# Kernel optimization log

Measured on AMD Instinct MI355X. Metric: run time of the kernel, lower is better.

Reference implementation:

```python
import jax, jax.numpy as jnp
import numpy as np
from jax import lax

B, N, FIN, T = 16, 1024, 32, 24
K, CC, CT = 3, 64, 64   # cheb order, nb_chev_filter, nb_time_filter
EPS = 1e-5


def setup_inputs() -> dict:
    key = jax.random.key(0)
    ks = jax.random.split(key, 16)
    g = lambda i, shape, sc=1.0: jax.random.normal(ks[i], shape, jnp.float32) * sc
    return dict(
        x=g(0, (B, N, FIN, T)),
        # spatial attention params
        W1=g(1, (T,), 0.1), W2=g(2, (FIN, T), 0.1), W3=g(3, (FIN,), 0.1),
        # temporal attention params
        U1=g(4, (N,), 0.03), U2=g(5, (FIN, N), 0.03), U3=g(6, (FIN,), 0.1),
        # Chebyshev polynomials T_k (K,N,N) and Theta (K,F_in,C_chev)
        cheb=g(7, (K, N, N), 1.0 / np.sqrt(N)),
        Theta=g(8, (K, FIN, CC), 1.0 / np.sqrt(FIN)),
        # time conv (1,3) stride (1,1) pad (0,1), residual conv (1,1)
        tc_w=g(9, (CT, CC, 1, 3), 1.0 / np.sqrt(3 * CC)), tc_b=g(10, (CT,), 0.01),
        rc_w=g(11, (CT, FIN, 1, 1), 1.0 / np.sqrt(FIN)), rc_b=g(12, (CT,), 0.01),
        gamma=jnp.ones((CT,), jnp.float32), beta=jnp.zeros((CT,), jnp.float32),
    )


def _layer_norm(z, gamma, beta):
    mu = jnp.mean(z, axis=-1, keepdims=True)
    var = jnp.mean(jnp.square(z - mu), axis=-1, keepdims=True)
    return (z - mu) * lax.rsqrt(var + EPS) * gamma + beta


def reference(x, W1, W2, W3, U1, U2, U3, cheb, Theta, tc_w, tc_b, rc_w, rc_b, gamma, beta):
    # ---- temporal attention: (B,T,T), softmax over axis=1 (as in torch dim=1)
    lhs_t = jnp.einsum('bnft,n->btf', x, U1) @ U2            # (B,T,N)
    rhs_t = jnp.einsum('f,bnft->bnt', U3, x)                 # (B,N,T)
    E = jax.nn.softmax(jnp.einsum('btn,bns->bts', lhs_t, rhs_t), axis=1)  # (B,T,T)

    # x_TAt = reshape(B,N*F,T) @ E, reshaped back
    x_TAt = jnp.einsum('bnft,bts->bnfs', x, E)               # (B,N,F,T)

    # ---- spatial attention on x_TAt: (B,N,N), softmax over axis=1
    lhs_s = jnp.einsum('bnft,t->bnf', x_TAt, W1) @ W2        # (B,N,T)
    rhs_s = jnp.einsum('f,bnft->btn', W3, x_TAt)             # (B,T,N)
    S = jax.nn.softmax(jnp.einsum('bnt,btm->bnm', lhs_s, rhs_s), axis=1)  # (B,N,N)

    # ---- K-order Chebyshev graph conv with spatial attention, fused over T and K
    # rhs[k,b,m,f,t] = sum_n (T_k[n,m]*S[b,n,m]) * x[b,n,f,t]
    Tk_at = cheb[:, None] * S[None]                          # (K,B,N,N)
    rhs = jnp.einsum('kbnm,bnft->kbmft', Tk_at, x)           # (K,B,N,F,T)
    spatial_gcn = jax.nn.relu(jnp.einsum('kbmft,kfo->bmot', rhs, Theta))  # (B,N,CC,T)

    # ---- time conv (1,3) pad (0,1) on (B,CC,N,T)
    dn = ('NCHW', 'OIHW', 'NCHW')
    tco = lax.conv_general_dilated(spatial_gcn.transpose(0, 2, 1, 3), tc_w,
                                   window_strides=(1, 1), padding=[(0, 0), (1, 1)],
                                   dimension_numbers=dn) + tc_b[None, :, None, None]
    # ---- residual 1x1 conv on (B,F,N,T)
    res = lax.conv_general_dilated(x.transpose(0, 2, 1, 3), rc_w,
                                   window_strides=(1, 1), padding=[(0, 0), (0, 0)],
                                   dimension_numbers=dn) + rc_b[None, :, None, None]

    z = jax.nn.relu(res + tco)                               # (B,CT,N,T)
    z = _layer_norm(z.transpose(0, 3, 2, 1), gamma, beta)    # (B,T,N,CT), LN over CT
    return z.transpose(0, 2, 3, 1)                           # (B,N,CT,T)
```

## Files before the change

### kernel.cpp

```cpp
#include <hip/hip_runtime.h>
#include <hip/hip_bf16.h>
#include <math.h>


namespace {

constexpr int B = 16, N = 1024, F = 32, T = 24, CC = 64, CT = 64;
constexpr int FT = F * T;
constexpr int CTT = CT * T;
constexpr int NSEG = 8;

using f32x4  = __attribute__((ext_vector_type(4))) float;
using short8 = __attribute__((ext_vector_type(8))) short;

__device__ __forceinline__ float b2f(__hip_bfloat16 v) { return __bfloat162float(v); }
__device__ __forceinline__ unsigned short f2bu(float x) {
  union { float f; unsigned u; } c; c.f = x;
  unsigned u = c.u;
  return (unsigned short)((u + 0x7FFFu + ((u >> 16) & 1u)) >> 16);
}
__device__ __forceinline__ float us2f(unsigned short u) {
  union { unsigned u; float f; } c; c.u = ((unsigned)u) << 16; return c.f;
}
__device__ __forceinline__ void gload16(const void* g, void* l) {
  __builtin_amdgcn_global_load_lds(
      (const __attribute__((address_space(1))) unsigned int*)g,
      (__attribute__((address_space(3))) unsigned int*)l, 16, 0, 0);
}

__global__ void k_lhs_t(const float* x, const float* U1, float* lhst) {
  int bi = blockIdx.x;
  int f = bi % F; int t = (bi / F) % T; int b = bi / (F * T);
  int tid = threadIdx.x;
  float acc = 0.f;
  for (int n = tid; n < N; n += 64)
    acc += x[(((size_t)b * N + n) * F + f) * T + t] * U1[n];
  #pragma unroll
  for (int off = 32; off > 0; off >>= 1) acc += __shfl_down(acc, off);
  if (tid == 0) lhst[bi] = acc;
}

__global__ void k_lhs2(const float* lhst, const float* U2, float* lhs2) {
  __shared__ float ls[F];
  int tid = threadIdx.x;
  int id = blockIdx.x * 256 + tid;
  int n = id % N; int bt = id / N;
  if (tid < F) ls[tid] = lhst[bt * F + tid];
  __syncthreads();
  float acc = 0.f;
  #pragma unroll
  for (int f = 0; f < F; ++f) acc += ls[f] * U2[f * N + n];
  lhs2[id] = acc;
}

__global__ void k_fx(const float* x, const float* U3, const float* W3,
                     float* rhst, float* w3x) {
  __shared__ float u3s[F], w3s[F];
  int tid = threadIdx.x;
  if (tid < F) { u3s[tid] = U3[tid]; w3s[tid] = W3[tid]; }
  __syncthreads();
  int id = blockIdx.x * 256 + tid;
  int t = id % T; int bn = id / T;
  float au = 0.f, aw = 0.f;
  #pragma unroll
  for (int f = 0; f < F; ++f) {
    float v = x[((size_t)bn * F + f) * T + t];
    au += u3s[f] * v; aw += w3s[f] * v;
  }
  rhst[id] = au; w3x[id] = aw;
}

__global__ void k_Elog(const float* lhs2, const float* rhst, float* Elog) {
  int bi = blockIdx.x;
  int s = bi % T; int t = (bi / T) % T; int b = bi / (T * T);
  int tid = threadIdx.x;
  float acc = 0.f;
  for (int n = tid; n < N; n += 64)
    acc += lhs2[(b * T + t) * N + n] * rhst[(b * N + n) * T + s];
  #pragma unroll
  for (int off = 32; off > 0; off >>= 1) acc += __shfl_down(acc, off);
  if (tid == 0) Elog[bi] = acc;
}

__global__ void k_Esm(const float* Elog, float* E) {
  int b = blockIdx.x; int s = threadIdx.x;
  if (s >= T) return;
  float mx = -1e30f;
  for (int t = 0; t < T; ++t) mx = fmaxf(mx, Elog[(b * T + t) * T + s]);
  float sum = 0.f;
  for (int t = 0; t < T; ++t) sum += expf(Elog[(b * T + t) * T + s] - mx);
  float inv = 1.f / sum;
  for (int t = 0; t < T; ++t)
    E[(b * T + t) * T + s] = expf(Elog[(b * T + t) * T + s] - mx) * inv;
}

__global__ void k_EW1(const float* E, const float* W1, float* EW1) {
  int b = blockIdx.x; int t = threadIdx.x;
  if (t >= T) return;
  float acc = 0.f;
  for (int s = 0; s < T; ++s) acc += E[(b * T + t) * T + s] * W1[s];
  EW1[b * T + t] = acc;
}

__global__ void k_tmp1x(const float* x, const float* EW1, float* tmp1) {
  __shared__ float ew[T];
  int tid = threadIdx.x;
  int id = blockIdx.x * 256 + tid;
  int b = id / (N * F);
  if (tid < T) ew[tid] = EW1[b * T + tid];
  __syncthreads();
  const float* xr = x + (size_t)id * T;
  float acc = 0.f;
  #pragma unroll
  for (int t = 0; t < T; ++t) acc += xr[t] * ew[t];
  tmp1[id] = acc;
}

__global__ void k_lhs_s(const float* tmp1, const float* W2, float* lhss) {
  int id = blockIdx.x * 256 + threadIdx.x;
  int t = id % T; int bn = id / T;
  float acc = 0.f;
  #pragma unroll
  for (int f = 0; f < F; ++f) acc += tmp1[bn * F + f] * W2[f * T + t];
  lhss[id] = acc;
}

__global__ void k_rhss(const float* w3x, const float* E, float* rhss) {
  __shared__ float Ec[T];
  int tid = threadIdx.x;
  int id = blockIdx.x * 256 + tid;
  int m = id % N; int t = (id / N) % T; int b = id / (N * T);
  if (tid < T) Ec[tid] = E[(b * T + tid) * T + t];
  __syncthreads();
  const float* wr = w3x + ((size_t)b * N + m) * T;
  float acc = 0.f;
  #pragma unroll
  for (int tp = 0; tp < T; ++tp) acc += wr[tp] * Ec[tp];
  rhss[id] = acc;
}

__global__ void k_Slog(const float* lhss, const float* rhss, __hip_bfloat16* S) {
  __shared__ float rt[T][256];
  __shared__ float lt[16][T];
  int m0 = blockIdx.x * 256, n0 = blockIdx.y * 16, b = blockIdx.z;
  int tid = threadIdx.x;
  for (int t = 0; t < T; ++t) rt[t][tid] = rhss[((size_t)b * T + t) * N + m0 + tid];
  for (int i = tid; i < 16 * T; i += 256) {
    int n = i / T, t = i % T;
    lt[n][t] = lhss[((size_t)b * N + n0 + n) * T + t];
  }
  __syncthreads();
  #pragma unroll 4
  for (int n = 0; n < 16; ++n) {
    float acc = 0.f;
    #pragma unroll
    for (int t = 0; t < T; ++t) acc += lt[n][t] * rt[t][tid];
    S[((size_t)b * N + n0 + n) * N + m0 + tid] = __float2bfloat16(acc);
  }
}

__global__ __launch_bounds__(256) void k_Ssum(const __hip_bfloat16* S,
                                              float* pmx, float* psm) {
  int m0 = blockIdx.x * 128; int b = blockIdx.y; int z = blockIdx.z;
  int tid = threadIdx.x;
  int lane = tid & 63, nq = tid >> 6;
  int c = m0 + lane * 2;
  float mx0 = -1e30f, sm0 = 0.f, mx1 = -1e30f, sm1 = 0.f;
  #pragma unroll 4
  for (int i = 0; i < 32; ++i) {
    int n = z * 128 + i * 4 + nq;
    unsigned u = *(const unsigned*)&S[((size_t)b * N + n) * N + c];
    float v0 = us2f((unsigned short)(u & 0xffffu));
    float v1 = us2f((unsigned short)(u >> 16));
    float nm0 = fmaxf(mx0, v0);
    sm0 = sm0 * __expf(mx0 - nm0) + __expf(v0 - nm0); mx0 = nm0;
    float nm1 = fmaxf(mx1, v1);
    sm1 = sm1 * __expf(mx1 - nm1) + __expf(v1 - nm1); mx1 = nm1;
  }
  __shared__ float lmx[4][128], lsm[4][128];
  lmx[nq][lane * 2] = mx0; lmx[nq][lane * 2 + 1] = mx1;
  lsm[nq][lane * 2] = sm0; lsm[nq][lane * 2 + 1] = sm1;
  __syncthreads();
  if (nq == 0) {
    #pragma unroll
    for (int cc2 = 0; cc2 < 2; ++cc2) {
      int col = lane * 2 + cc2;
      float M = lmx[0][col], Sg = lsm[0][col];
      #pragma unroll
      for (int s = 1; s < 4; ++s) {
        float m2 = lmx[s][col], s2 = lsm[s][col];
        float nm = fmaxf(M, m2);
        Sg = Sg * __expf(M - nm) + s2 * __expf(m2 - nm);
        M = nm;
      }
      pmx[((size_t)z * B + b) * N + m0 + col] = M;
      psm[((size_t)z * B + b) * N + m0 + col] = Sg;
    }
  }
}

__global__ void k_Scomb(const float* pmx, const float* psm,
                        float* smax, float* sinv) {
  int id = blockIdx.x * 256 + threadIdx.x;
  float M = -1e30f, Sg = 0.f;
  #pragma unroll
  for (int z = 0; z < NSEG; ++z) {
    float m2 = pmx[(size_t)z * B * N + id];
    float s2 = psm[(size_t)z * B * N + id];
    float nm = fmaxf(M, m2);
    Sg = Sg * __expf(M - nm) + s2 * __expf(m2 - nm);
    M = nm;
  }
  smax[id] = M;
  sinv[id] = 1.f / Sg;
}

__global__ __launch_bounds__(256) void k_prepA(const float* cheb,
                                               const __hip_bfloat16* S,
                                               const float* smax,
                                               const float* sinv,
                                               unsigned short* Abf,
                                               int Bc, int b0) {
  __shared__ float Tl[64][65];
  int z = blockIdx.z;
  int k = z / Bc, bl = z % Bc, b = b0 + bl;
  int n0 = blockIdx.x * 64, m0 = blockIdx.y * 64;
  int tid = threadIdx.x;
  int j = tid & 63, i4 = tid >> 6;
  float cm = smax[(size_t)b * N + m0 + j];
  float ci = sinv[(size_t)b * N + m0 + j];
  #pragma unroll
  for (int it = 0; it < 16; ++it) {
    int i = it * 4 + i4;
    Tl[i][j] = cheb[((size_t)k * N + n0 + i) * N + m0 + j] *
               (__expf(b2f(S[((size_t)b * N + n0 + i) * N + m0 + j]) - cm) * ci);
  }
  __syncthreads();
  int i2 = (tid & 31) * 2, j8 = tid >> 5;
  #pragma unroll
  for (int it = 0; it < 8; ++it) {
    int jj = it * 8 + j8;
    unsigned u = (unsigned)f2bu(Tl[i2][jj]) | ((unsigned)f2bu(Tl[i2 + 1][jj]) << 16);
    *(unsigned*)&Abf[((size_t)z * N + m0 + jj) * N + n0 + i2] = u;
  }
}

__global__ __launch_bounds__(256) void k_prepX(const float* x, unsigned short* xT,
                                               int b0) {
  __shared__ float Tl[64][65];
  int bl = blockIdx.z, b = b0 + bl;
  int n0 = blockIdx.x * 64, c0 = blockIdx.y * 64;
  int tid = threadIdx.x;
  int j = tid & 63, i4 = tid >> 6;
  #pragma unroll
  for (int it = 0; it < 16; ++it) {
    int i = it * 4 + i4;
    Tl[i][j] = x[((size_t)b * N + n0 + i) * FT + c0 + j];
  }
  __syncthreads();
  int i2 = (tid & 31) * 2, j8 = tid >> 5;
  #pragma unroll
  for (int it = 0; it < 8; ++it) {
    int jj = it * 8 + j8;
    int c = c0 + jj;
    int row = (c % 24) * 32 + c / 24;
    unsigned u = (unsigned)f2bu(Tl[i2][jj]) | ((unsigned)f2bu(Tl[i2 + 1][jj]) << 16);
    *(unsigned*)&xT[((size_t)bl * FT + row) * N + n0 + i2] = u;
  }
}

__global__ void k_prepW(const float* Theta, const float* tcw, const float* rcw,
                        unsigned short* wbf) {
  int tid = threadIdx.x;
  for (int g = tid; g < 64 * 96; g += 256) {
    int o = g / 96, kk = g % 96;
    wbf[g] = f2bu(Theta[kk * 64 + o]);
  }
  for (int g = tid; g < 64 * 192; g += 256) {
    int o = g / 192, r = g % 192;
    int jj = r / 64, cc = r % 64;
    wbf[6144 + g] = f2bu(tcw[o * 192 + cc * 3 + jj]);
  }
  for (int g = tid; g < 32 * 64; g += 256) {
    int f = g >> 6, o = g & 63;
    wbf[18432 + (f >> 1) * 128 + o * 2 + (f & 1)] = f2bu(rcw[o * 32 + f]);
  }
}

__global__ __launch_bounds__(256) void k_gemm3(const unsigned short* Abf,
                                               const unsigned short* xT,
                                               float* rk, size_t kstride,
                                               int Bc) {
  __shared__ __align__(16) unsigned short A_l[3 * 64 * 64];
  __shared__ __align__(16) unsigned short X_l[128 * 64];
  int bl = blockIdx.z;
  int m0 = blockIdx.y * 64, c0 = blockIdx.x * 128;
  int tid = threadIdx.x;
  int lane = tid & 63, w = tid >> 6;
  int l15 = lane & 15, quad = lane >> 4;
  int wmi = w & 1, wci = w >> 1;
  int nh = lane & 7, ml = lane >> 3;
  int swz = nh ^ ml;

  f32x4 acc[3][2][4];
  #pragma unroll
  for (int k = 0; k < 3; ++k)
    #pragma unroll
    for (int mt = 0; mt < 2; ++mt)
      #pragma unroll
      for (int ct = 0; ct < 4; ++ct) acc[k][mt][ct] = (f32x4){0.f, 0.f, 0.f, 0.f};

  for (int n0 = 0; n0 < N; n0 += 64) {
    #pragma unroll
    for (int it = 0; it < 6; ++it) {
      int k = it >> 1, mh = it & 1;
      int rowb = mh * 32 + w * 8;
      gload16(&Abf[((size_t)(k * Bc + bl) * N + m0 + rowb + ml) * N + n0 + swz * 8],
              &A_l[(k * 64 + rowb) * 64]);
    }
    #pragma unroll
    for (int it = 0; it < 4; ++it) {
      int cb = it * 32 + w * 8;
      gload16(&xT[((size_t)bl * FT + c0 + cb + ml) * N + n0 + swz * 8],
              &X_l[cb * 64]);
    }
    __syncthreads();
    #pragma unroll
    for (int ks = 0; ks < 2; ++ks) {
      short8 bfr[4];
      #pragma unroll
      for (int ct = 0; ct < 4; ++ct) {
        int row = wci * 64 + ct * 16 + l15;
        int pc = (ks * 4 + quad) ^ (row & 7);
        bfr[ct] = *(const short8*)&X_l[row * 64 + pc * 8];
      }
      #pragma unroll
      for (int k = 0; k < 3; ++k)
        #pragma unroll
        for (int mt = 0; mt < 2; ++mt) {
          int row = wmi * 32 + mt * 16 + l15;
          int pc = (ks * 4 + quad) ^ (row & 7);
          short8 af = *(const short8*)&A_l[(k * 64 + row) * 64 + pc * 8];
          #pragma unroll
          for (int ct = 0; ct < 4; ++ct)
            acc[k][mt][ct] = __builtin_amdgcn_mfma_f32_16x16x32_bf16(
                af, bfr[ct], acc[k][mt][ct], 0, 0, 0);
        }
    }
    __syncthreads();
  }
  #pragma unroll
  for (int k = 0; k < 3; ++k)
    #pragma unroll
    for (int mt = 0; mt < 2; ++mt)
      #pragma unroll
      for (int ct = 0; ct < 4; ++ct) {
        int col = c0 + wci * 64 + ct * 16 + l15;
        #pragma unroll
        for (int r = 0; r < 4; ++r) {
          int row = m0 + wmi * 32 + mt * 16 + quad * 4 + r;
          rk[k * kstride + ((size_t)bl * N + row) * FT + col] = acc[k][mt][ct][r];
        }
      }
}

__global__ __launch_bounds__(256) void k_fuse(const float* rk, size_t kstride,
                                              const float* x,
                                              const unsigned short* wbf,
                                              const float* tcb, const float* rcb,
                                              const float* gam, const float* bet,
                                              float* out, int b0) {
  __shared__ __align__(16) unsigned char smem[38272];
  unsigned short* A_l = (unsigned short*)smem;
  float* co_l = (float*)(smem + 13312);
  int tid = threadIdx.x;
  int w = tid >> 6, lane = tid & 63;
  int l15 = lane & 15, quad = lane >> 4;
  int r0l = blockIdx.x * 4;
  int o0 = w * 16;

  short8 bth[3], btc[6];
  {
    int o = o0 + l15;
    #pragma unroll
    for (int ks = 0; ks < 3; ++ks)
      bth[ks] = *(const short8*)&wbf[o * 96 + ks * 32 + quad * 8];
    #pragma unroll
    for (int s = 0; s < 6; ++s)
      btc[s] = *(const short8*)&wbf[6144 + o * 192 + s * 32 + quad * 8];
  }

  #pragma unroll
  for (int it = 0; it < 9; ++it) {
    int ch = it * 256 + tid;
    int k = ch / 768, r2 = ch % 768;
    int m = r2 / 192, r3 = r2 % 192;
    int t = r3 >> 3, fq = r3 & 7;
    const float4 v = *(const float4*)&rk[(size_t)k * kstride +
        (size_t)(r0l + m) * FT + t * 32 + fq * 4];
    unsigned long long pk = (unsigned long long)f2bu(v.x) |
        ((unsigned long long)f2bu(v.y) << 16) |
        ((unsigned long long)f2bu(v.z) << 32) |
        ((unsigned long long)f2bu(v.w) << 48);
    *(unsigned long long*)&A_l[(m * 24 + t) * 104 + k * 32 + fq * 4] = pk;
  }
  __syncthreads();

  f32x4 th[6];
  #pragma unroll
  for (int Mt = 0; Mt < 6; ++Mt) {
    th[Mt] = (f32x4){0.f, 0.f, 0.f, 0.f};
    #pragma unroll
    for (int ks = 0; ks < 3; ++ks) {
      short8 af = *(const short8*)&A_l[(Mt * 16 + l15) * 104 + ks * 32 + quad * 8];
      th[Mt] = __builtin_amdgcn_mfma_f32_16x16x32_bf16(af, bth[ks], th[Mt], 0, 0, 0);
    }
  }
  __syncthreads();

  #pragma unroll
  for (int e = tid; e < 512; e += 256) {
    int m = e >> 7, rr = (e >> 6) & 1, cc = e & 63;
    int rp = m * 26 + rr * 25;
    *(unsigned short*)(smem + rp * 128 + ((cc * 2) ^ ((rp & 7) << 4))) = 0;
  }
  #pragma unroll
  for (int Mt = 0; Mt < 6; ++Mt)
    #pragma unroll
    for (int r = 0; r < 4; ++r) {
      int row = Mt * 16 + quad * 4 + r;
      int m = row / 24, t = row % 24;
      int rp = m * 26 + t + 1;
      int cc = o0 + l15;
      *(unsigned short*)(smem + rp * 128 + ((cc * 2) ^ ((rp & 7) << 4))) =
          f2bu(fmaxf(th[Mt][r], 0.f));
    }
  __syncthreads();

  f32x4 cv[6];
  #pragma unroll
  for (int Mt = 0; Mt < 6; ++Mt) {
    int row = Mt * 16 + l15;
    int m = row / 24, t = row % 24;
    cv[Mt] = (f32x4){0.f, 0.f, 0.f, 0.f};
    #pragma unroll
    for (int s = 0; s < 6; ++s) {
      int rp = m * 26 + t + (s >> 1);
      int cb = (32 * (s & 1) + quad * 8) * 2;
      short8 af = *(const short8*)(smem + rp * 128 + (cb ^ ((rp & 7) << 4)));
      cv[Mt] = __builtin_amdgcn_mfma_f32_16x16x32_bf16(af, btc[s], cv[Mt], 0, 0, 0);
    }
  }
  #pragma unroll
  for (int Mt = 0; Mt < 6; ++Mt)
    #pragma unroll
    for (int r = 0; r < 4; ++r) {
      int row = Mt * 16 + quad * 4 + r;
      co_l[row * 65 + o0 + l15] = cv[Mt][r];
    }
  __syncthreads();

  int o = lane;
  float bias = tcb[o] + rcb[o];
  float acc[T];
  #pragma unroll
  for (int t = 0; t < T; ++t) acc[t] = co_l[(w * 24 + t) * 65 + o] + bias;

  size_t grow = (size_t)b0 * N + r0l + w;
  const float* xrow = x + grow * FT;
  const unsigned* rcp = (const unsigned*)(wbf + 18432);
  #pragma unroll 4
  for (int f2 = 0; f2 < 16; ++f2) {
    unsigned u = rcp[f2 * 64 + o];
    float wf0 = us2f((unsigned short)(u & 0xffffu));
    float wf1 = us2f((unsigned short)(u >> 16));
    const float4* xp0 = (const float4*)&xrow[(f2 * 2) * 24];
    const float4* xp1 = (const float4*)&xrow[(f2 * 2 + 1) * 24];
    #pragma unroll
    for (int q = 0; q < 6; ++q) {
      float4 v0 = xp0[q], v1 = xp1[q];
      acc[q * 4 + 0] += wf0 * v0.x + wf1 * v1.x;
      acc[q * 4 + 1] += wf0 * v0.y + wf1 * v1.y;
      acc[q * 4 + 2] += wf0 * v0.z + wf1 * v1.z;
      acc[q * 4 + 3] += wf0 * v0.w + wf1 * v1.w;
    }
  }
  float g = gam[o], be = bet[o];
  #pragma unroll
  for (int t = 0; t < T; ++t) {
    float z = fmaxf(acc[t], 0.f);
    float s = z, q = z * z;
    #pragma unroll
    for (int off = 1; off < 64; off <<= 1) {
      s += __shfl_xor(s, off);
      q += __shfl_xor(q, off);
    }
    float mu = s * (1.f / 64.f);
    float var = q * (1.f / 64.f) - mu * mu;
    acc[t] = (z - mu) * rsqrtf(var + 1e-5f) * g + be;
  }
  float* orow = out + grow * CTT + o * T;
  #pragma unroll
  for (int q = 0; q < 6; ++q)
    ((float4*)orow)[q] =
        make_float4(acc[q * 4], acc[q * 4 + 1], acc[q * 4 + 2], acc[q * 4 + 3]);
}

}

extern "C" void kernel_launch(void* const* d_in, const int* in_sizes, int n_in,
                              void* d_out, int out_size, void* d_ws, size_t ws_size,
                              hipStream_t stream) {
  (void)in_sizes; (void)n_in; (void)out_size;
  const float* x     = (const float*)d_in[0];
  const float* W1    = (const float*)d_in[1];
  const float* W2    = (const float*)d_in[2];
  const float* W3    = (const float*)d_in[3];
  const float* U1    = (const float*)d_in[4];
  const float* U2    = (const float*)d_in[5];
  const float* U3    = (const float*)d_in[6];
  const float* cheb  = (const float*)d_in[7];
  const float* Theta = (const float*)d_in[8];
  const float* tcw   = (const float*)d_in[9];
  const float* tcb   = (const float*)d_in[10];
  const float* rcw   = (const float*)d_in[11];
  const float* rcb   = (const float*)d_in[12];
  const float* gam   = (const float*)d_in[13];
  const float* bet   = (const float*)d_in[14];
  float* out = (float*)d_out;

  const size_t SB_BYTES = (size_t)B * N * N * 2;
  const size_t WB_BYTES = 65536;
  const size_t AB_PER_B = (size_t)3 * N * N * 2;
  const size_t XT_PER_B = (size_t)FT * N * 2;
  const size_t RK_PER_B = (size_t)3 * N * FT * 4;
  const size_t SMALL = 2816384 * 4;
  int Bc = 16;
  while (Bc > 1 && SB_BYTES + WB_BYTES + SMALL +
             (size_t)Bc * (AB_PER_B + XT_PER_B + RK_PER_B) > ws_size)
    Bc >>= 1;

  char* w = (char*)d_ws;
  __hip_bfloat16* Sb = (__hip_bfloat16*)w;
  unsigned short* wbf = (unsigned short*)(w + SB_BYTES);
  unsigned short* Abf = (unsigned short*)(w + SB_BYTES + WB_BYTES);
  unsigned short* xTb = (unsigned short*)(w + SB_BYTES + WB_BYTES +
                                          (size_t)Bc * AB_PER_B);
  float* rkbuf = (float*)(w + SB_BYTES + WB_BYTES +
                          (size_t)Bc * (AB_PER_B + XT_PER_B));
  size_t kstride = (size_t)Bc * N * FT;
  float* sm = (float*)(w + SB_BYTES + WB_BYTES +
                       (size_t)Bc * (AB_PER_B + XT_PER_B + RK_PER_B));
  float* lhst = sm;
  float* lhs2 = lhst + B * T * F;
  float* rhst = lhs2 + B * T * N;
  float* w3x  = rhst + B * N * T;
  float* Elog = w3x + B * N * T;
  float* E    = Elog + B * T * T;
  float* EW1  = E + B * T * T;
  float* tmp1 = EW1 + B * T;
  float* lhss = tmp1 + B * N * F;
  float* rhss = lhss + B * N * T;
  float* pmx  = rhss + B * N * T;
  float* psm  = pmx + NSEG * B * N;
  float* smax = psm + NSEG * B * N;
  float* sinv = smax + B * N;

  k_lhs_t<<<B * T * F, 64, 0, stream>>>(x, U1, lhst);
  k_lhs2<<<(B * T * N) / 256, 256, 0, stream>>>(lhst, U2, lhs2);
  k_fx<<<(B * N * T) / 256, 256, 0, stream>>>(x, U3, W3, rhst, w3x);
  k_Elog<<<B * T * T, 64, 0, stream>>>(lhs2, rhst, Elog);
  k_Esm<<<B, 64, 0, stream>>>(Elog, E);
  k_EW1<<<B, 64, 0, stream>>>(E, W1, EW1);

  k_tmp1x<<<(B * N * F) / 256, 256, 0, stream>>>(x, EW1, tmp1);
  k_lhs_s<<<(B * N * T) / 256, 256, 0, stream>>>(tmp1, W2, lhss);
  k_rhss<<<(B * N * T) / 256, 256, 0, stream>>>(w3x, E, rhss);
  k_Slog<<<dim3(N / 256, N / 16, B), 256, 0, stream>>>(lhss, rhss, Sb);
  k_Ssum<<<dim3(N / 128, B, NSEG), 256, 0, stream>>>(Sb, pmx, psm);
  k_Scomb<<<(B * N) / 256, 256, 0, stream>>>(pmx, psm, smax, sinv);

  k_prepW<<<1, 256, 0, stream>>>(Theta, tcw, rcw, wbf);

  for (int b0 = 0; b0 < B; b0 += Bc) {
    k_prepA<<<dim3(N / 64, N / 64, 3 * Bc), 256, 0, stream>>>(cheb, Sb, smax,
                                                              sinv, Abf, Bc, b0);
    k_prepX<<<dim3(N / 64, FT / 64, Bc), 256, 0, stream>>>(x, xTb, b0);
    k_gemm3<<<dim3(FT / 128, N / 64, Bc), 256, 0, stream>>>(Abf, xTb, rkbuf,
                                                            kstride, Bc);
    k_fuse<<<Bc * N / 4, 256, 0, stream>>>(rkbuf, kstride, x, wbf, tcb, rcb,
                                           gam, bet, out, b0);
  }
}
```

Measured before the change: 682.9 us.

## Fuse Theta projection and ReLU into Chebyshev GEMM epilogue, store bf16 intermediate

The Chebyshev GEMM epilogue now stages its three K outputs in shared memory as bf16 and immediately applies the Theta projection with MFMA plus ReLU. It writes a bf16 (N,T,CC) spatial-GCN tensor instead of three fp32 (N,F*T) buffers. The tail kernel then only loads this smaller intermediate for the time conv, residual and layernorm. This removes a large fp32 global write and read round trip, at the cost of more shared memory and register pressure in the GEMM kernel.

```diff
diff --git a/kernel.cpp b/kernel.cpp
--- a/kernel.cpp
+++ b/kernel.cpp
@@ -289,12 +289,16 @@
 
 __global__ __launch_bounds__(256) void k_gemm3(const unsigned short* Abf,
                                                const unsigned short* xT,
-                                               float* rk, size_t kstride,
+                                               const unsigned short* wbf,
+                                               unsigned short* sg,
                                                int Bc) {
-  __shared__ __align__(16) unsigned short A_l[3 * 64 * 64];
-  __shared__ __align__(16) unsigned short X_l[128 * 64];
+  __shared__ __align__(16) unsigned char smem[53248];
+  unsigned short* A_l  = (unsigned short*)smem;
+  unsigned short* X_l  = (unsigned short*)(smem + 24576);
+  unsigned short* A_th = (unsigned short*)smem;
   int bl = blockIdx.z;
   int m0 = blockIdx.y * 64, c0 = blockIdx.x * 128;
+  int t0 = blockIdx.x * 4;
   int tid = threadIdx.x;
   int lane = tid & 63, w = tid >> 6;
   int l15 = lane & 15, quad = lane >> 4;
@@ -349,29 +353,58 @@
     }
     __syncthreads();
   }
+
+  short8 bth[4][3];
+  #pragma unroll
+  for (int ot = 0; ot < 4; ++ot)
+    #pragma unroll
+    for (int ks = 0; ks < 3; ++ks)
+      bth[ot][ks] = *(const short8*)&wbf[(ot * 16 + l15) * 96 + ks * 32 + quad * 8];
+
   #pragma unroll
   for (int k = 0; k < 3; ++k)
     #pragma unroll
     for (int mt = 0; mt < 2; ++mt)
       #pragma unroll
       for (int ct = 0; ct < 4; ++ct) {
-        int col = c0 + wci * 64 + ct * 16 + l15;
+        int tl = wci * 2 + (ct >> 1);
+        int f  = (ct & 1) * 16 + l15;
         #pragma unroll
         for (int r = 0; r < 4; ++r) {
-          int row = m0 + wmi * 32 + mt * 16 + quad * 4 + r;
-          rk[k * kstride + ((size_t)bl * N + row) * FT + col] = acc[k][mt][ct][r];
+          int mloc = wmi * 32 + mt * 16 + quad * 4 + r;
+          A_th[(mloc * 4 + tl) * 104 + k * 32 + f] = f2bu(acc[k][mt][ct][r]);
         }
       }
-}
-
-__global__ __launch_bounds__(256) void k_fuse(const float* rk, size_t kstride,
+  __syncthreads();
+
+  #pragma unroll
+  for (int i = 0; i < 4; ++i) {
+    short8 af[3];
+    #pragma unroll
+    for (int ks = 0; ks < 3; ++ks)
+      af[ks] = *(const short8*)&A_th[((w * 4 + i) * 16 + l15) * 104 + ks * 32 + quad * 8];
+    int mloc = (w * 4 + i) * 4 + quad;
+    size_t base = ((size_t)(bl * N + m0 + mloc)) * (T * CC) + (size_t)t0 * CC;
+    #pragma unroll
+    for (int ot = 0; ot < 4; ++ot) {
+      f32x4 th = (f32x4){0.f, 0.f, 0.f, 0.f};
+      #pragma unroll
+      for (int ks = 0; ks < 3; ++ks)
+        th = __builtin_amdgcn_mfma_f32_16x16x32_bf16(af[ks], bth[ot][ks], th, 0, 0, 0);
+      #pragma unroll
+      for (int rr = 0; rr < 4; ++rr)
+        sg[base + (size_t)rr * CC + ot * 16 + l15] = f2bu(fmaxf(th[rr], 0.f));
+    }
+  }
+}
+
+__global__ __launch_bounds__(256) void k_tail(const unsigned short* sg,
                                               const float* x,
                                               const unsigned short* wbf,
                                               const float* tcb, const float* rcb,
                                               const float* gam, const float* bet,
                                               float* out, int b0) {
   __shared__ __align__(16) unsigned char smem[38272];
-  unsigned short* A_l = (unsigned short*)smem;
   float* co_l = (float*)(smem + 13312);
   int tid = threadIdx.x;
   int w = tid >> 6, lane = tid & 63;
@@ -379,62 +412,29 @@
   int r0l = blockIdx.x * 4;
   int o0 = w * 16;
 
-  short8 bth[3], btc[6];
+  short8 btc[6];
   {
     int o = o0 + l15;
     #pragma unroll
-    for (int ks = 0; ks < 3; ++ks)
-      bth[ks] = *(const short8*)&wbf[o * 96 + ks * 32 + quad * 8];
-    #pragma unroll
     for (int s = 0; s < 6; ++s)
       btc[s] = *(const short8*)&wbf[6144 + o * 192 + s * 32 + quad * 8];
   }
 
-  #pragma unroll
-  for (int it = 0; it < 9; ++it) {
+  if (tid < 64) {
+    int m = tid >> 4, rr = (tid >> 3) & 1, ck = tid & 7;
+    int rp = m * 26 + rr * 25;
+    *(uint4*)(smem + rp * 128 + ((ck * 16) ^ ((rp & 7) << 4))) =
+        make_uint4(0, 0, 0, 0);
+  }
+  #pragma unroll
+  for (int it = 0; it < 3; ++it) {
     int ch = it * 256 + tid;
-    int k = ch / 768, r2 = ch % 768;
-    int m = r2 / 192, r3 = r2 % 192;
-    int t = r3 >> 3, fq = r3 & 7;
-    const float4 v = *(const float4*)&rk[(size_t)k * kstride +
-        (size_t)(r0l + m) * FT + t * 32 + fq * 4];
-    unsigned long long pk = (unsigned long long)f2bu(v.x) |
-        ((unsigned long long)f2bu(v.y) << 16) |
-        ((unsigned long long)f2bu(v.z) << 32) |
-        ((unsigned long long)f2bu(v.w) << 48);
-    *(unsigned long long*)&A_l[(m * 24 + t) * 104 + k * 32 + fq * 4] = pk;
-  }
-  __syncthreads();
-
-  f32x4 th[6];
-  #pragma unroll
-  for (int Mt = 0; Mt < 6; ++Mt) {
-    th[Mt] = (f32x4){0.f, 0.f, 0.f, 0.f};
-    #pragma unroll
-    for (int ks = 0; ks < 3; ++ks) {
-      short8 af = *(const short8*)&A_l[(Mt * 16 + l15) * 104 + ks * 32 + quad * 8];
-      th[Mt] = __builtin_amdgcn_mfma_f32_16x16x32_bf16(af, bth[ks], th[Mt], 0, 0, 0);
-    }
-  }
-  __syncthreads();
-
-  #pragma unroll
-  for (int e = tid; e < 512; e += 256) {
-    int m = e >> 7, rr = (e >> 6) & 1, cc = e & 63;
-    int rp = m * 26 + rr * 25;
-    *(unsigned short*)(smem + rp * 128 + ((cc * 2) ^ ((rp & 7) << 4))) = 0;
-  }
-  #pragma unroll
-  for (int Mt = 0; Mt < 6; ++Mt)
-    #pragma unroll
-    for (int r = 0; r < 4; ++r) {
-      int row = Mt * 16 + quad * 4 + r;
-      int m = row / 24, t = row % 24;
-      int rp = m * 26 + t + 1;
-      int cc = o0 + l15;
-      *(unsigned short*)(smem + rp * 128 + ((cc * 2) ^ ((rp & 7) << 4))) =
-          f2bu(fmaxf(th[Mt][r], 0.f));
-    }
+    int m = ch / 192, rem = ch % 192;
+    int t = rem >> 3, ck = rem & 7;
+    uint4 v = *(const uint4*)&sg[((size_t)(r0l + m)) * (T * CC) + t * CC + ck * 8];
+    int rp = m * 26 + t + 1;
+    *(uint4*)(smem + rp * 128 + ((ck * 16) ^ ((rp & 7) << 4))) = v;
+  }
   __syncthreads();
 
   f32x4 cv[6];
@@ -533,11 +533,11 @@
   const size_t WB_BYTES = 65536;
   const size_t AB_PER_B = (size_t)3 * N * N * 2;
   const size_t XT_PER_B = (size_t)FT * N * 2;
-  const size_t RK_PER_B = (size_t)3 * N * FT * 4;
+  const size_t SG_PER_B = (size_t)N * T * CC * 2;
   const size_t SMALL = 2816384 * 4;
   int Bc = 16;
   while (Bc > 1 && SB_BYTES + WB_BYTES + SMALL +
-             (size_t)Bc * (AB_PER_B + XT_PER_B + RK_PER_B) > ws_size)
+             (size_t)Bc * (AB_PER_B + XT_PER_B + SG_PER_B) > ws_size)
     Bc >>= 1;
 
   char* w = (char*)d_ws;
@@ -546,11 +546,10 @@
   unsigned short* Abf = (unsigned short*)(w + SB_BYTES + WB_BYTES);
   unsigned short* xTb = (unsigned short*)(w + SB_BYTES + WB_BYTES +
                                           (size_t)Bc * AB_PER_B);
-  float* rkbuf = (float*)(w + SB_BYTES + WB_BYTES +
-                          (size_t)Bc * (AB_PER_B + XT_PER_B));
-  size_t kstride = (size_t)Bc * N * FT;
+  unsigned short* sgb = (unsigned short*)(w + SB_BYTES + WB_BYTES +
+                                          (size_t)Bc * (AB_PER_B + XT_PER_B));
   float* sm = (float*)(w + SB_BYTES + WB_BYTES +
-                       (size_t)Bc * (AB_PER_B + XT_PER_B + RK_PER_B));
+                       (size_t)Bc * (AB_PER_B + XT_PER_B + SG_PER_B));
   float* lhst = sm;
   float* lhs2 = lhst + B * T * F;
   float* rhst = lhs2 + B * T * N;
@@ -586,9 +585,9 @@
     k_prepA<<<dim3(N / 64, N / 64, 3 * Bc), 256, 0, stream>>>(cheb, Sb, smax,
                                                               sinv, Abf, Bc, b0);
     k_prepX<<<dim3(N / 64, FT / 64, Bc), 256, 0, stream>>>(x, xTb, b0);
-    k_gemm3<<<dim3(FT / 128, N / 64, Bc), 256, 0, stream>>>(Abf, xTb, rkbuf,
-                                                            kstride, Bc);
-    k_fuse<<<Bc * N / 4, 256, 0, stream>>>(rkbuf, kstride, x, wbf, tcb, rcb,
+    k_gemm3<<<dim3(FT / 128, N / 64, Bc), 256, 0, stream>>>(Abf, xTb, wbf,
+                                                            sgb, Bc);
+    k_tail<<<Bc * N / 4, 256, 0, stream>>>(sgb, x, wbf, tcb, rcb,
                                            gam, bet, out, b0);
   }
 }
```

Result: no change. 690.6 us (+1.1%).
